# Kernel tuning notes

Hardware: AMD Instinct MI355X
Metric: run time of the kernel (lower is better)

## Reference

```python
import jax, jax.numpy as jnp
import numpy as np
from jax import lax

B, C_IN, N, C_OUT, K = 16, 128, 2048, 256, 20
EPS = 1e-5


def setup_inputs() -> dict:
    key = jax.random.key(0)
    k1, k2 = jax.random.split(key)
    x = jax.random.normal(k1, (B, C_IN, N), dtype=jnp.float32)
    W = jax.random.normal(k2, (C_OUT, 2 * C_IN), dtype=jnp.float32) * (1.0 / np.sqrt(2 * C_IN))
    gamma = jnp.ones((C_OUT,), dtype=jnp.float32)
    beta = jnp.zeros((C_OUT,), dtype=jnp.float32)
    return {"x": x, "W": W, "gamma": gamma, "beta": beta, "k": K}


def _knn_inds(x, k):
    # squared pairwise distance: (B, N, N); computed with no grad (stop_gradient)
    xs = lax.stop_gradient(x)
    inner = jnp.einsum('bcn,bcm->bnm', xs, xs)
    sq = jnp.sum(xs * xs, axis=1)  # (B, N)
    pd = sq[:, :, None] - 2.0 * inner + sq[:, None, :]
    _, inds = lax.top_k(-pd, k)  # smallest distances -> (B, N, k)
    return inds


def reference(x, W, gamma, beta, k):
    knn = _knn_inds(x, k)                                   # (B, N, k) int
    # gather neighbours: neigh[b,c,n,j] = x[b,c,knn[b,n,j]]
    neigh = jax.vmap(lambda xb, kb: xb[:, kb])(x, knn)      # (B, C, N, k)
    central = jnp.broadcast_to(x[:, :, :, None], neigh.shape)
    edge = jnp.concatenate([central, neigh - central], axis=1)  # (B, 2C, N, k)
    # 1x1 conv (bias-free) as GEMM
    y = jnp.einsum('oc,bcnk->bonk', W, edge)                # (B, C_out, N, k)
    # BatchNorm2d (training-mode batch stats) + affine
    mean = jnp.mean(y, axis=(0, 2, 3), keepdims=True)
    var = jnp.var(y, axis=(0, 2, 3), keepdims=True)
    y = (y - mean) * lax.rsqrt(var + EPS)
    y = y * gamma[None, :, None, None] + beta[None, :, None, None]
    y = jax.nn.relu(y)
    return jnp.max(y, axis=3)                               # (B, C_out, N)
```

## Files before the change

### kernel.cpp

```cpp
#include <hip/hip_runtime.h>

#define B_   16
#define CIN  128
#define NPT  2048
#define COUT 256
#define KNN  20
#define KEEP 16
#define CAND 64
#define SIFT 32
#define EPS  1e-5f
#define DBIAS 256.0f

#define SQ_OFF   0ull
#define IDX_OFF  131072ull
#define UT_OFF   2752512ull
#define VT_OFF   36306944ull
#define GS_OFF   69861376ull
#define ST_OFF   69865472ull
#define AMAX_OFF 69871616ull
#define AMIN_OFF 103426048ull
#define WS_NEED_FUSED 136980480ull
#define XT_OFF   UT_OFF
#define XHT_OFF  VT_OFF

typedef _Float16 f16x8 __attribute__((ext_vector_type(8)));
typedef float    f32x4 __attribute__((ext_vector_type(4)));

__global__ __launch_bounds__(256) void prep_kernel(const float* __restrict__ x,
                                                   float* __restrict__ xT,
                                                   _Float16* __restrict__ xhT,
                                                   float* __restrict__ sqh) {
    __shared__ float Ls[128 * 68];
    __shared__ float ps[4 * 64];
    const int b = blockIdx.y, n0 = blockIdx.x * 64, t = threadIdx.x;
    const float* xb = x + (size_t)b * CIN * NPT;
    #pragma unroll
    for (int e = 0; e < 8; ++e) {
        int f = e * 256 + t;
        int c = f >> 4, n4 = (f & 15) << 2;
        *(float4*)&Ls[c * 68 + n4] = *(const float4*)&xb[(size_t)c * NPT + n0 + n4];
    }
    __syncthreads();
    {
        int nl = t & 63, part = t >> 6;
        float acc = 0.f;
        #pragma unroll
        for (int j = 0; j < 32; ++j) {
            float vh = (float)(_Float16)Ls[(part * 32 + j) * 68 + nl];
            acc += vh * vh;
        }
        ps[part * 64 + nl] = acc;
    }
    #pragma unroll
    for (int e = 0; e < 2; ++e) {
        int u = e * 256 + t;
        int nl = u >> 3, ck = (u & 7) << 4;
        float vv[16];
        #pragma unroll
        for (int j = 0; j < 16; ++j) vv[j] = Ls[(ck + j) * 68 + nl];
        size_t row = (size_t)b * NPT + n0 + nl;
        #pragma unroll
        for (int j = 0; j < 4; ++j) {
            float4 w = {vv[4 * j], vv[4 * j + 1], vv[4 * j + 2], vv[4 * j + 3]};
            *(float4*)&xT[row * CIN + ck + 4 * j] = w;
        }
        f16x8 h0, h1;
        #pragma unroll
        for (int j = 0; j < 8; ++j) { h0[j] = (_Float16)vv[j]; h1[j] = (_Float16)vv[8 + j]; }
        *(f16x8*)&xhT[row * CIN + ck] = h0;
        *(f16x8*)&xhT[row * CIN + ck + 8] = h1;
    }
    __syncthreads();
    if (t < 64) sqh[b * NPT + n0 + t] = ps[t] + ps[64 + t] + ps[128 + t] + ps[192 + t];
}

__global__ void wconv_kernel(const float* __restrict__ W,
                             _Float16* __restrict__ Wu,
                             _Float16* __restrict__ Wv) {
    int gid = blockIdx.x * 256 + threadIdx.x;
    int o = gid >> 7, c = gid & 127;
    float w1 = W[o * 256 + c], w2 = W[o * 256 + 128 + c];
    Wu[gid] = (_Float16)(w1 - w2);
    Wv[gid] = (_Float16)w2;
}

__device__ __forceinline__ void stage_pts(const _Float16* __restrict__ xhb,
                                          _Float16* buf, int base_n, int t) {
    const int l15 = t & 15, ks = t >> 6;
    const int quad = (t >> 4) & 3;
    const int c = ks * 32 + quad * 8;
    #pragma unroll
    for (int e = 0; e < 4; ++e) {
        const int n = base_n + e * 16 + l15;
        const _Float16* src = xhb + (size_t)n * CIN + c;
        _Float16* dst = buf + (size_t)(e * 256 + (t & 192)) * 8;
        __builtin_amdgcn_global_load_lds(
            (const __attribute__((address_space(1))) void*)src,
            (__attribute__((address_space(3))) void*)dst, 16, 0, 0);
    }
}

__global__ __launch_bounds__(256, 2) void knn_kernel(const _Float16* __restrict__ xhT,
                                                     const float* __restrict__ xT,
                                                     const float* __restrict__ sqh,
                                                     int* __restrict__ knn_out) {
    __shared__ char smraw[58368];
    _Float16* bufA = (_Float16*)smraw;
    _Float16* bufB = (_Float16*)(smraw + 16384);
    float*    Dt   = (float*)(smraw + 32768);
    float*    sqm  = (float*)(smraw + 50176);

    const int b  = blockIdx.y;
    const int q0 = blockIdx.x * 64;
    const int t  = threadIdx.x;
    const int lane = t & 63, wv = t >> 6;
    const int l15 = lane & 15, quad = lane >> 4;
    const _Float16* xhb = xhT + (size_t)b * NPT * CIN;

    #pragma unroll
    for (int e = 0; e < 8; ++e)
        sqm[e * 256 + t] = sqh[b * NPT + e * 256 + t] + DBIAS;

    stage_pts(xhb, bufA, q0, t);
    __syncthreads();
    f16x8 af[4];
    #pragma unroll
    for (int ks = 0; ks < 4; ++ks)
        af[ks] = *(const f16x8*)(bufA + (size_t)((wv * 4 + ks) * 64 + lane) * 8);
    stage_pts(xhb, bufB, 0, t);

    float bd[KEEP];
    #pragma unroll
    for (int i = 0; i < KEEP; ++i) bd[i] = 3.0e38f;
    const int qi = t >> 2, r = t & 3;

    #pragma unroll 1
    for (int s = 0; s < 32; ++s) {
        __syncthreads();
        _Float16* cur = (s & 1) ? bufA : bufB;
        if (s < 31) stage_pts(xhb, (s & 1) ? bufB : bufA, (s + 1) * 64, t);
        const int m0 = s * 64;
        f32x4 acc[4];
        #pragma unroll
        for (int mt4 = 0; mt4 < 4; ++mt4) acc[mt4] = (f32x4){0.f, 0.f, 0.f, 0.f};
        #pragma unroll
        for (int ks = 0; ks < 4; ++ks) {
            #pragma unroll
            for (int mt4 = 0; mt4 < 4; ++mt4) {
                f16x8 bf = *(const f16x8*)(cur + (size_t)((mt4 * 4 + ks) * 64 + lane) * 8);
                acc[mt4] = __builtin_amdgcn_mfma_f32_16x16x32_f16(af[ks], bf, acc[mt4], 0, 0, 0);
            }
        }
        #pragma unroll
        for (int mt4 = 0; mt4 < 4; ++mt4) {
            float sm_ = sqm[m0 + mt4 * 16 + l15];
            #pragma unroll
            for (int reg = 0; reg < 4; ++reg) {
                int q = wv * 16 + quad * 4 + reg;
                Dt[q * 68 + mt4 * 16 + l15] = sm_ - 2.f * acc[mt4][reg];
            }
        }
        __syncthreads();
        float nk[16];
        #pragma unroll
        for (int i = 0; i < 16; ++i) {
            unsigned bb = __float_as_uint(Dt[qi * 68 + (i << 2) + r]);
            nk[i] = __uint_as_float((bb & 0xFFFFF800u) | (unsigned)(m0 + (i << 2) + r));
        }
        #pragma unroll
        for (int kk = 2; kk <= 16; kk <<= 1) {
            #pragma unroll
            for (int j = kk >> 1; j > 0; j >>= 1) {
                #pragma unroll
                for (int i = 0; i < 16; ++i) {
                    int p = i ^ j;
                    if (p > i) {
                        float a = nk[i], c = nk[p];
                        float lo = fminf(a, c), hi = fmaxf(a, c);
                        if ((i & kk) == 0) { nk[i] = lo; nk[p] = hi; }
                        else               { nk[i] = hi; nk[p] = lo; }
                    }
                }
            }
        }
        #pragma unroll
        for (int i = 0; i < 16; ++i) bd[i] = fminf(bd[i], nk[15 - i]);
        #pragma unroll
        for (int j = 8; j > 0; j >>= 1) {
            #pragma unroll
            for (int i = 0; i < 16; ++i) {
                int p = i ^ j;
                if (p > i) {
                    float a = bd[i], c = bd[p];
                    bd[i] = fminf(a, c);
                    bd[p] = fmaxf(a, c);
                }
            }
        }
    }

    float* Keys = (float*)smraw;
    int*   Surv = (int*)(smraw + 16640);
    double* ddL = (double*)(smraw + 25088);
    #pragma unroll
    for (int i = 0; i < KEEP; ++i)
        Keys[qi * 65 + r * KEEP + i] = bd[i];
    __syncthreads();
    {
        int cnt[KEEP];
        #pragma unroll
        for (int i = 0; i < KEEP; ++i) cnt[i] = 0;
        #pragma unroll 4
        for (int j = 0; j < CAND; ++j) {
            float kj = Keys[qi * 65 + j];
            #pragma unroll
            for (int i = 0; i < KEEP; ++i)
                cnt[i] += (kj < bd[i]) ? 1 : 0;
        }
        __syncthreads();
        #pragma unroll
        for (int i = 0; i < KEEP; ++i)
            if (cnt[i] < SIFT)
                Surv[qi * 33 + cnt[i]] = (int)(__float_as_uint(bd[i]) & 0x7FFu);
    }
    __syncthreads();

    int ms[8];
    #pragma unroll
    for (int k = 0; k < 8; ++k) ms[k] = Surv[qi * 33 + r * 8 + k] & 2047;
    double dd8[8];
    #pragma unroll
    for (int k = 0; k < 8; ++k) dd8[k] = 0.0;
    const float* xTb = xT + (size_t)b * NPT * CIN;
    const float* qrow = xTb + (size_t)(q0 + qi) * CIN;
    #pragma unroll 1
    for (int ch = 0; ch < 8; ++ch) {
        double qd[16];
        #pragma unroll
        for (int j = 0; j < 4; ++j) {
            float4 qv = *(const float4*)&qrow[ch * 16 + 4 * j];
            qd[4 * j] = (double)qv.x; qd[4 * j + 1] = (double)qv.y;
            qd[4 * j + 2] = (double)qv.z; qd[4 * j + 3] = (double)qv.w;
        }
        #pragma unroll
        for (int k = 0; k < 8; ++k) {
            const float* mrow = xTb + (size_t)ms[k] * CIN + ch * 16;
            float4 ma = *(const float4*)&mrow[0];
            float4 mb = *(const float4*)&mrow[4];
            float4 mc = *(const float4*)&mrow[8];
            float4 md = *(const float4*)&mrow[12];
            double ss = dd8[k], d0;
            d0 = qd[0]  - (double)ma.x; ss = fma(d0, d0, ss);
            d0 = qd[1]  - (double)ma.y; ss = fma(d0, d0, ss);
            d0 = qd[2]  - (double)ma.z; ss = fma(d0, d0, ss);
            d0 = qd[3]  - (double)ma.w; ss = fma(d0, d0, ss);
            d0 = qd[4]  - (double)mb.x; ss = fma(d0, d0, ss);
            d0 = qd[5]  - (double)mb.y; ss = fma(d0, d0, ss);
            d0 = qd[6]  - (double)mb.z; ss = fma(d0, d0, ss);
            d0 = qd[7]  - (double)mb.w; ss = fma(d0, d0, ss);
            d0 = qd[8]  - (double)mc.x; ss = fma(d0, d0, ss);
            d0 = qd[9]  - (double)mc.y; ss = fma(d0, d0, ss);
            d0 = qd[10] - (double)mc.z; ss = fma(d0, d0, ss);
            d0 = qd[11] - (double)mc.w; ss = fma(d0, d0, ss);
            d0 = qd[12] - (double)md.x; ss = fma(d0, d0, ss);
            d0 = qd[13] - (double)md.y; ss = fma(d0, d0, ss);
            d0 = qd[14] - (double)md.z; ss = fma(d0, d0, ss);
            d0 = qd[15] - (double)md.w; ss = fma(d0, d0, ss);
            dd8[k] = ss;
        }
    }

    #pragma unroll
    for (int k = 0; k < 8; ++k) ddL[qi * 33 + r * 8 + k] = dd8[k];
    __syncthreads();
    int* dst = knn_out + ((size_t)b * NPT + q0 + qi) * KNN;
    #pragma unroll
    for (int k = 0; k < 8; ++k) {
        int c = 0;
        #pragma unroll 4
        for (int j = 0; j < SIFT; ++j)
            c += (ddL[qi * 33 + j] < dd8[k]) ? 1 : 0;
        if (c < KNN) dst[c] = ms[k];
    }
}

__global__ __launch_bounds__(256) void uv_gemm_h(const _Float16* __restrict__ xhT,
                                                 const _Float16* __restrict__ Wu,
                                                 const _Float16* __restrict__ Wv,
                                                 float* __restrict__ uT,
                                                 float* __restrict__ vT) {
    __shared__ _Float16 Bx[8192];
    const int b = blockIdx.y, n0 = blockIdx.x * 64, t = threadIdx.x;
    const int lane = t & 63, w = t >> 6, l15 = lane & 15, quad = lane >> 4;
    stage_pts(xhT + (size_t)b * NPT * CIN, Bx, n0, t);
    __syncthreads();
    f16x8 bf[4];
    #pragma unroll
    for (int ks = 0; ks < 4; ++ks)
        bf[ks] = *(const f16x8*)(Bx + (size_t)((w * 4 + ks) * 64 + lane) * 8);
    const int n = n0 + w * 16 + l15;
    #pragma unroll 1
    for (int ot = 0; ot < 16; ++ot) {
        const _Float16* wu = Wu + (size_t)(ot * 16 + l15) * 128 + quad * 8;
        const _Float16* wv2 = Wv + (size_t)(ot * 16 + l15) * 128 + quad * 8;
        f32x4 au = (f32x4){0.f, 0.f, 0.f, 0.f};
        f32x4 av = (f32x4){0.f, 0.f, 0.f, 0.f};
        #pragma unroll
        for (int ks = 0; ks < 4; ++ks) {
            f16x8 a_u = *(const f16x8*)(wu + ks * 32);
            f16x8 a_v = *(const f16x8*)(wv2 + ks * 32);
            au = __builtin_amdgcn_mfma_f32_16x16x32_f16(a_u, bf[ks], au, 0, 0, 0);
            av = __builtin_amdgcn_mfma_f32_16x16x32_f16(a_v, bf[ks], av, 0, 0, 0);
        }
        size_t base = ((size_t)b * NPT + n) * COUT + ot * 16 + quad * 4;
        *(f32x4*)&uT[base] = au;
        *(f32x4*)&vT[base] = av;
    }
}

__global__ __launch_bounds__(256) void uv_gemm(const float* __restrict__ x,
                                               const float* __restrict__ W,
                                               float* __restrict__ uT,
                                               float* __restrict__ vT) {
    __shared__ float Ax[32 * 64];
    __shared__ float Bu[32 * 68];
    __shared__ float Bv[32 * 68];
    const int b  = blockIdx.z;
    const int n0 = blockIdx.x * 64;
    const int o0 = blockIdx.y * 64;
    const int t  = threadIdx.x;
    const int tx = t & 15, ty = t >> 4;
    const float* xb = x + (size_t)b * CIN * NPT;
    float au[4][4], av_[4][4];
    #pragma unroll
    for (int i = 0; i < 4; ++i)
        #pragma unroll
        for (int j = 0; j < 4; ++j) { au[i][j] = 0.f; av_[i][j] = 0.f; }
    #pragma unroll 1
    for (int kc = 0; kc < 4; ++kc) {
        const int c0 = kc * 32;
        __syncthreads();
        #pragma unroll
        for (int e = 0; e < 2; ++e) {
            int f = e * 256 + t;
            int cz = f >> 4, ni = (f & 15) << 2;
            *(float4*)&Ax[(cz << 6) + ni] = *(const float4*)&xb[(size_t)(c0 + cz) * NPT + n0 + ni];
        }
        #pragma unroll
        for (int e = 0; e < 8; ++e) {
            int ii = e * 256 + t;
            int cz = ii & 31, oj = ii >> 5;
            float w1 = W[(size_t)(o0 + oj) * 256 + c0 + cz];
            float w2 = W[(size_t)(o0 + oj) * 256 + 128 + c0 + cz];
            Bu[cz * 68 + oj] = w1 - w2;
            Bv[cz * 68 + oj] = w2;
        }
        __syncthreads();
        #pragma unroll 8
        for (int cz = 0; cz < 32; ++cz) {
            const float4 a4 = *(const float4*)&Ax[(cz << 6) + (tx << 2)];
            float bu0 = Bu[cz * 68 + (ty << 2) + 0], bv0 = Bv[cz * 68 + (ty << 2) + 0];
            float bu1 = Bu[cz * 68 + (ty << 2) + 1], bv1 = Bv[cz * 68 + (ty << 2) + 1];
            float bu2 = Bu[cz * 68 + (ty << 2) + 2], bv2 = Bv[cz * 68 + (ty << 2) + 2];
            float bu3 = Bu[cz * 68 + (ty << 2) + 3], bv3 = Bv[cz * 68 + (ty << 2) + 3];
            au[0][0] += a4.x * bu0; au[0][1] += a4.x * bu1; au[0][2] += a4.x * bu2; au[0][3] += a4.x * bu3;
            au[1][0] += a4.y * bu0; au[1][1] += a4.y * bu1; au[1][2] += a4.y * bu2; au[1][3] += a4.y * bu3;
            au[2][0] += a4.z * bu0; au[2][1] += a4.z * bu1; au[2][2] += a4.z * bu2; au[2][3] += a4.z * bu3;
            au[3][0] += a4.w * bu0; au[3][1] += a4.w * bu1; au[3][2] += a4.w * bu2; au[3][3] += a4.w * bu3;
            av_[0][0] += a4.x * bv0; av_[0][1] += a4.x * bv1; av_[0][2] += a4.x * bv2; av_[0][3] += a4.x * bv3;
            av_[1][0] += a4.y * bv0; av_[1][1] += a4.y * bv1; av_[1][2] += a4.y * bv2; av_[1][3] += a4.y * bv3;
            av_[2][0] += a4.z * bv0; av_[2][1] += a4.z * bv1; av_[2][2] += a4.z * bv2; av_[2][3] += a4.z * bv3;
            av_[3][0] += a4.w * bv0; av_[3][1] += a4.w * bv1; av_[3][2] += a4.w * bv2; av_[3][3] += a4.w * bv3;
        }
    }
    #pragma unroll
    for (int i = 0; i < 4; ++i) {
        int n = n0 + (tx << 2) + i;
        size_t base = ((size_t)b * NPT + n) * COUT + o0 + (ty << 2);
        float4 u4 = {au[i][0], au[i][1], au[i][2], au[i][3]};
        float4 v4 = {av_[i][0], av_[i][1], av_[i][2], av_[i][3]};
        *(float4*)&uT[base] = u4;
        *(float4*)&vT[base] = v4;
    }
}

__global__ __launch_bounds__(256) void gather_stats(const float* __restrict__ uT,
                                                    const float* __restrict__ vT,
                                                    const int* __restrict__ knn_in,
                                                    double* __restrict__ gsum,
                                                    float* __restrict__ aMax,
                                                    float* __restrict__ aMin) {
    __shared__ int sidx[16 * KNN];
    const int b  = blockIdx.y;
    const int n0 = blockIdx.x * 64 + blockIdx.z * 16;
    const int o  = threadIdx.x;
    for (int e = o; e < 16 * KNN; e += 256)
        sidx[e] = knn_in[((size_t)b * NPT + n0) * KNN + e];
    __syncthreads();
    const float* ub = uT + ((size_t)b * NPT + n0) * COUT + o;
    const float* vb = vT + (size_t)b * NPT * COUT + o;
    float* amx = aMax + ((size_t)b * NPT + n0) * COUT + o;
    float* amn = aMin + ((size_t)b * NPT + n0) * COUT + o;
    double s1 = 0.0, s2 = 0.0;
    #pragma unroll 1
    for (int s = 0; s < 16; ++s) {
        float u = ub[(size_t)s * COUT];
        float vmax = -3e38f, vmin = 3e38f, vsum = 0.f, vsq = 0.f;
        #pragma unroll
        for (int j = 0; j < KNN; ++j) {
            float v = vb[(size_t)sidx[s * KNN + j] * COUT];
            vmax = fmaxf(vmax, v);
            vmin = fminf(vmin, v);
            vsum += v;
            vsq = fmaf(v, v, vsq);
        }
        s1 += 20.0 * (double)u + (double)vsum;
        s2 += 20.0 * (double)u * (double)u + 2.0 * (double)u * (double)vsum + (double)vsq;
        amx[(size_t)s * COUT] = vmax;
        amn[(size_t)s * COUT] = vmin;
    }
    atomicAdd(&gsum[o], s1);
    atomicAdd(&gsum[COUT + o], s2);
}

__global__ __launch_bounds__(256) void stats_kernel(const float* __restrict__ uT,
                                                    const float* __restrict__ vT,
                                                    const int* __restrict__ knn_in,
                                                    double* __restrict__ gsum) {
    __shared__ int sidx[64 * KNN];
    const int b  = blockIdx.y;
    const int n0 = blockIdx.x * 64;
    const int o  = threadIdx.x;
    for (int e = o; e < 64 * KNN; e += 256)
        sidx[e] = knn_in[((size_t)b * NPT + n0) * KNN + e];
    __syncthreads();
    const float* ub = uT + ((size_t)b * NPT + n0) * COUT + o;
    const float* vb = vT + (size_t)b * NPT * COUT + o;
    double s1 = 0.0, s2 = 0.0;
    #pragma unroll 1
    for (int s = 0; s < 64; ++s) {
        float u = ub[(size_t)s * COUT];
        #pragma unroll
        for (int j = 0; j < KNN; ++j) {
            float y = u + vb[(size_t)sidx[s * KNN + j] * COUT];
            s1 += (double)y;
            s2 = fma((double)y, (double)y, s2);
        }
    }
    atomicAdd(&gsum[o], s1);
    atomicAdd(&gsum[COUT + o], s2);
}

__global__ void finalize_kernel(const double* __restrict__ gsum,
                                const float* __restrict__ gamma,
                                const float* __restrict__ beta,
                                float* __restrict__ st) {
    const int o = threadIdx.x;
    const double M = (double)B_ * NPT * KNN;
    double mean = gsum[o] / M;
    double var  = gsum[COUT + o] / M - mean * mean;
    float inv = 1.0f / sqrtf((float)var + EPS);
    float s = gamma[o] * inv;
    st[o] = s;
    st[COUT + o] = beta[o] - (float)mean * s;
}

__global__ __launch_bounds__(256, 2) void out2_kernel(const float* __restrict__ uT,
                                                      const float* __restrict__ aMax,
                                                      const float* __restrict__ aMin,
                                                      const float* __restrict__ st,
                                                      float* __restrict__ out) {
    __shared__ float zt[256 * 68];
    const int b  = blockIdx.y;
    const int n0 = blockIdx.x * 64;
    const int o  = threadIdx.x;
    const float s  = st[o];
    const float tt = st[COUT + o];
    const float* ub  = uT   + ((size_t)b * NPT + n0) * COUT + o;
    const float* amx = aMax + ((size_t)b * NPT + n0) * COUT + o;
    const float* amn = aMin + ((size_t)b * NPT + n0) * COUT + o;
    #pragma unroll 2
    for (int si = 0; si < 64; ++si) {
        float u = ub[(size_t)si * COUT];
        float y1 = u + amx[(size_t)si * COUT];
        float y2 = u + amn[(size_t)si * COUT];
        float z1 = fmaxf(s * y1 + tt, 0.f);
        float z2 = fmaxf(s * y2 + tt, 0.f);
        zt[o * 68 + si] = fmaxf(z1, z2);
    }
    __syncthreads();
    float* dst = out + ((size_t)b * COUT + o) * NPT + n0;
    #pragma unroll
    for (int i = 0; i < 16; ++i)
        *(float4*)&dst[i * 4] = *(const float4*)&zt[o * 68 + i * 4];
}

__global__ __launch_bounds__(256, 2) void out_kernel(const float* __restrict__ uT,
                                                     const float* __restrict__ vT,
                                                     const int* __restrict__ knn_in,
                                                     const float* __restrict__ st,
                                                     float* __restrict__ out) {
    __shared__ int sidx[64 * KNN];
    __shared__ float zt[256 * 68];
    const int b  = blockIdx.y;
    const int n0 = blockIdx.x * 64;
    const int o  = threadIdx.x;
    for (int e = o; e < 64 * KNN; e += 256)
        sidx[e] = knn_in[((size_t)b * NPT + n0) * KNN + e];
    __syncthreads();
    const float s  = st[o];
    const float tt = st[COUT + o];
    const float* ub = uT + ((size_t)b * NPT + n0) * COUT + o;
    const float* vb = vT + (size_t)b * NPT * COUT + o;
    #pragma unroll 1
    for (int si = 0; si < 64; ++si) {
        float u = ub[(size_t)si * COUT];
        float ymax = -3e38f, ymin = 3e38f;
        #pragma unroll
        for (int j = 0; j < KNN; ++j) {
            float y = u + vb[(size_t)sidx[si * KNN + j] * COUT];
            ymax = fmaxf(ymax, y);
            ymin = fminf(ymin, y);
        }
        float z1 = fmaxf(s * ymax + tt, 0.f);
        float z2 = fmaxf(s * ymin + tt, 0.f);
        zt[o * 68 + si] = fmaxf(z1, z2);
    }
    __syncthreads();
    float* dst = out + ((size_t)b * COUT + o) * NPT + n0;
    #pragma unroll
    for (int i = 0; i < 16; ++i)
        *(float4*)&dst[i * 4] = *(const float4*)&zt[o * 68 + i * 4];
}

extern "C" void kernel_launch(void* const* d_in, const int* in_sizes, int n_in,
                              void* d_out, int out_size, void* d_ws, size_t ws_size,
                              hipStream_t stream) {
    const float* x     = (const float*)d_in[0];
    const float* W     = (const float*)d_in[1];
    const float* gamma = (const float*)d_in[2];
    const float* beta  = (const float*)d_in[3];
    float* out = (float*)d_out;
    char* ws = (char*)d_ws;
    float*     sqh  = (float*)(ws + SQ_OFF);
    int*       idx  = (int*)(ws + IDX_OFF);
    float*     uT   = (float*)(ws + UT_OFF);
    float*     vT   = (float*)(ws + VT_OFF);
    double*    gsum = (double*)(ws + GS_OFF);
    float*     st   = (float*)(ws + ST_OFF);
    float*     aMax = (float*)(ws + AMAX_OFF);
    float*     aMin = (float*)(ws + AMIN_OFF);
    const bool fused = (ws_size >= WS_NEED_FUSED);

    hipMemsetAsync(gsum, 0, 2 * COUT * sizeof(double), stream);
    if (fused) {
        float*    xT  = (float*)(ws + AMAX_OFF);
        _Float16* xhT = (_Float16*)(ws + AMAX_OFF + 16777216ull);
        _Float16* Wu  = (_Float16*)(ws + AMAX_OFF + 25165824ull);
        _Float16* Wv  = (_Float16*)(ws + AMAX_OFF + 25231360ull);
        prep_kernel<<<dim3(32, 16), 256, 0, stream>>>(x, xT, xhT, sqh);
        wconv_kernel<<<128, 256, 0, stream>>>(W, Wu, Wv);
        knn_kernel<<<dim3(32, 16), 256, 0, stream>>>(xhT, xT, sqh, idx);
        uv_gemm_h<<<dim3(32, 16), 256, 0, stream>>>(xhT, Wu, Wv, uT, vT);
        gather_stats<<<dim3(32, 16, 4), 256, 0, stream>>>(uT, vT, idx, gsum, aMax, aMin);
        finalize_kernel<<<1, 256, 0, stream>>>(gsum, gamma, beta, st);
        out2_kernel<<<dim3(32, 16), 256, 0, stream>>>(uT, aMax, aMin, st, out);
    } else {
        float*    xT  = (float*)(ws + XT_OFF);
        _Float16* xhT = (_Float16*)(ws + XHT_OFF);
        prep_kernel<<<dim3(32, 16), 256, 0, stream>>>(x, xT, xhT, sqh);
        knn_kernel<<<dim3(32, 16), 256, 0, stream>>>(xhT, xT, sqh, idx);
        uv_gemm<<<dim3(32, 4, 16), 256, 0, stream>>>(x, W, uT, vT);
        stats_kernel<<<dim3(32, 16), 256, 0, stream>>>(uT, vT, idx, gsum);
        finalize_kernel<<<1, 256, 0, stream>>>(gsum, gamma, beta, st);
        out_kernel<<<dim3(32, 16), 256, 0, stream>>>(uT, vT, idx, st, out);
    }
}
```

Measured before the change: 357.9 us.

## Make KNN distance tiles wave-private to remove block barriers in main loop

Each wave now keeps all 64 query fragments in registers and streams its own 16-candidate slice of points into a private double-buffered LDS region. Distances are written to a per-wave scratch tile, and each lane sorts its own query's 16 candidates. This removes the two __syncthreads per iteration and the shared 64-wide staging. The cost is more registers for the A fragments (64 VGPRs of f16x8), explicit waitcnt and sched barriers, and a changed candidate-to-thread mapping in the merge phase.

After: 352.2 us. Within noise of the previous version (-1.6%).

```diff
diff --git a/kernel.cpp b/kernel.cpp
--- a/kernel.cpp
+++ b/kernel.cpp
@@ -25,6 +25,7 @@
 
 typedef _Float16 f16x8 __attribute__((ext_vector_type(8)));
 typedef float    f32x4 __attribute__((ext_vector_type(4)));
+typedef float    f32x2 __attribute__((ext_vector_type(2)));
 
 __global__ __launch_bounds__(256) void prep_kernel(const float* __restrict__ x,
                                                    float* __restrict__ xT,
@@ -100,15 +101,24 @@
     }
 }
 
+__device__ __forceinline__ void stage_tile16(const _Float16* __restrict__ srcl,
+                                             _Float16* dsthalf) {
+    #pragma unroll
+    for (int e = 0; e < 4; ++e) {
+        __builtin_amdgcn_global_load_lds(
+            (const __attribute__((address_space(1))) void*)(srcl + e * 32),
+            (__attribute__((address_space(3))) void*)(dsthalf + (size_t)e * 512),
+            16, 0, 0);
+    }
+}
+
 __global__ __launch_bounds__(256, 2) void knn_kernel(const _Float16* __restrict__ xhT,
                                                      const float* __restrict__ xT,
                                                      const float* __restrict__ sqh,
                                                      int* __restrict__ knn_out) {
-    __shared__ char smraw[58368];
+    __shared__ char smraw[59392];
     _Float16* bufA = (_Float16*)smraw;
-    _Float16* bufB = (_Float16*)(smraw + 16384);
-    float*    Dt   = (float*)(smraw + 32768);
-    float*    sqm  = (float*)(smraw + 50176);
+    float*    sqm  = (float*)(smraw + 18432);
 
     const int b  = blockIdx.y;
     const int q0 = blockIdx.x * 64;
@@ -123,49 +133,68 @@
 
     stage_pts(xhb, bufA, q0, t);
     __syncthreads();
-    f16x8 af[4];
-    #pragma unroll
-    for (int ks = 0; ks < 4; ++ks)
-        af[ks] = *(const f16x8*)(bufA + (size_t)((wv * 4 + ks) * 64 + lane) * 8);
-    stage_pts(xhb, bufB, 0, t);
+
+    f16x8 af[4][4];
+    #pragma unroll
+    for (int qh = 0; qh < 4; ++qh)
+        #pragma unroll
+        for (int ks = 0; ks < 4; ++ks)
+            af[qh][ks] = *(const f16x8*)(bufA + (size_t)((qh * 4 + ks) * 64 + lane) * 8);
+    __syncthreads();
+
+    _Float16* wbuf = (_Float16*)(smraw + 26624 + wv * 8192);
+    float*    DtW  = (float*)(smraw + wv * 4608);
+    const _Float16* srcl = xhb + (size_t)(wv * 16 + l15) * CIN + quad * 8;
+
+    stage_tile16(srcl, wbuf);
 
     float bd[KEEP];
     #pragma unroll
     for (int i = 0; i < KEEP; ++i) bd[i] = 3.0e38f;
-    const int qi = t >> 2, r = t & 3;
 
     #pragma unroll 1
-    for (int s = 0; s < 32; ++s) {
-        __syncthreads();
-        _Float16* cur = (s & 1) ? bufA : bufB;
-        if (s < 31) stage_pts(xhb, (s & 1) ? bufB : bufA, (s + 1) * 64, t);
-        const int m0 = s * 64;
+    for (int ss = 0; ss < 32; ++ss) {
+        const int mb = ss * 64 + wv * 16;
+        asm volatile("s_waitcnt vmcnt(0)" ::: "memory");
+        __builtin_amdgcn_sched_barrier(0);
+        const _Float16* cur = wbuf + (ss & 1) * 2048;
+        f16x8 bf[4];
+        #pragma unroll
+        for (int ks = 0; ks < 4; ++ks)
+            bf[ks] = *(const f16x8*)(cur + ks * 512 + quad * 128 + l15 * 8);
+        float sm_ = sqm[mb + l15];
+        asm volatile("s_waitcnt lgkmcnt(0)" ::: "memory");
+        __builtin_amdgcn_sched_barrier(0);
+        if (ss < 31)
+            stage_tile16(srcl + (size_t)(ss + 1) * 64 * CIN,
+                         wbuf + ((ss + 1) & 1) * 2048);
+        __builtin_amdgcn_sched_barrier(0);
         f32x4 acc[4];
         #pragma unroll
-        for (int mt4 = 0; mt4 < 4; ++mt4) acc[mt4] = (f32x4){0.f, 0.f, 0.f, 0.f};
-        #pragma unroll
-        for (int ks = 0; ks < 4; ++ks) {
+        for (int qh = 0; qh < 4; ++qh) acc[qh] = (f32x4){0.f, 0.f, 0.f, 0.f};
+        #pragma unroll
+        for (int ks = 0; ks < 4; ++ks)
             #pragma unroll
-            for (int mt4 = 0; mt4 < 4; ++mt4) {
-                f16x8 bf = *(const f16x8*)(cur + (size_t)((mt4 * 4 + ks) * 64 + lane) * 8);
-                acc[mt4] = __builtin_amdgcn_mfma_f32_16x16x32_f16(af[ks], bf, acc[mt4], 0, 0, 0);
+            for (int qh = 0; qh < 4; ++qh)
+                acc[qh] = __builtin_amdgcn_mfma_f32_16x16x32_f16(af[qh][ks], bf[ks], acc[qh], 0, 0, 0);
+        const unsigned om = (unsigned)(mb + l15);
+        #pragma unroll
+        for (int qh = 0; qh < 4; ++qh) {
+            #pragma unroll
+            for (int rg = 0; rg < 4; ++rg) {
+                int q = qh * 16 + quad * 4 + rg;
+                float d = sm_ - 2.f * acc[qh][rg];
+                DtW[q * 18 + l15] = __uint_as_float((__float_as_uint(d) & 0xFFFFF800u) | om);
             }
         }
-        #pragma unroll
-        for (int mt4 = 0; mt4 < 4; ++mt4) {
-            float sm_ = sqm[m0 + mt4 * 16 + l15];
+        float nk[16];
+        {
+            const float* myrow = DtW + lane * 18;
             #pragma unroll
-            for (int reg = 0; reg < 4; ++reg) {
-                int q = wv * 16 + quad * 4 + reg;
-                Dt[q * 68 + mt4 * 16 + l15] = sm_ - 2.f * acc[mt4][reg];
+            for (int p = 0; p < 8; ++p) {
+                f32x2 v = *(const f32x2*)(myrow + 2 * p);
+                nk[2 * p] = v[0]; nk[2 * p + 1] = v[1];
             }
-        }
-        __syncthreads();
-        float nk[16];
-        #pragma unroll
-        for (int i = 0; i < 16; ++i) {
-            unsigned bb = __float_as_uint(Dt[qi * 68 + (i << 2) + r]);
-            nk[i] = __uint_as_float((bb & 0xFFFFF800u) | (unsigned)(m0 + (i << 2) + r));
         }
         #pragma unroll
         for (int kk = 2; kk <= 16; kk <<= 1) {
@@ -199,12 +228,14 @@
         }
     }
 
-    float* Keys = (float*)smraw;
-    int*   Surv = (int*)(smraw + 16640);
-    double* ddL = (double*)(smraw + 25088);
+    __syncthreads();
+
+    float*  Keys = (float*)smraw;
+    int*    Surv = (int*)(smraw + 16640);
+    double* ddL  = (double*)(smraw + 25088);
     #pragma unroll
     for (int i = 0; i < KEEP; ++i)
-        Keys[qi * 65 + r * KEEP + i] = bd[i];
+        Keys[lane * 65 + wv * KEEP + i] = bd[i];
     __syncthreads();
     {
         int cnt[KEEP];
@@ -212,7 +243,7 @@
         for (int i = 0; i < KEEP; ++i) cnt[i] = 0;
         #pragma unroll 4
         for (int j = 0; j < CAND; ++j) {
-            float kj = Keys[qi * 65 + j];
+            float kj = Keys[lane * 65 + j];
             #pragma unroll
             for (int i = 0; i < KEEP; ++i)
                 cnt[i] += (kj < bd[i]) ? 1 : 0;
@@ -221,18 +252,18 @@
         #pragma unroll
         for (int i = 0; i < KEEP; ++i)
             if (cnt[i] < SIFT)
-                Surv[qi * 33 + cnt[i]] = (int)(__float_as_uint(bd[i]) & 0x7FFu);
+                Surv[lane * 33 + cnt[i]] = (int)(__float_as_uint(bd[i]) & 0x7FFu);
     }
     __syncthreads();
 
     int ms[8];
     #pragma unroll
-    for (int k = 0; k < 8; ++k) ms[k] = Surv[qi * 33 + r * 8 + k] & 2047;
+    for (int k = 0; k < 8; ++k) ms[k] = Surv[lane * 33 + wv * 8 + k] & 2047;
     double dd8[8];
     #pragma unroll
     for (int k = 0; k < 8; ++k) dd8[k] = 0.0;
     const float* xTb = xT + (size_t)b * NPT * CIN;
-    const float* qrow = xTb + (size_t)(q0 + qi) * CIN;
+    const float* qrow = xTb + (size_t)(q0 + lane) * CIN;
     #pragma unroll 1
     for (int ch = 0; ch < 8; ++ch) {
         double qd[16];
@@ -246,40 +277,40 @@
         for (int k = 0; k < 8; ++k) {
             const float* mrow = xTb + (size_t)ms[k] * CIN + ch * 16;
             float4 ma = *(const float4*)&mrow[0];
-            float4 mb = *(const float4*)&mrow[4];
+            float4 mb2 = *(const float4*)&mrow[4];
             float4 mc = *(const float4*)&mrow[8];
             float4 md = *(const float4*)&mrow[12];
             double ss = dd8[k], d0;
-            d0 = qd[0]  - (double)ma.x; ss = fma(d0, d0, ss);
-            d0 = qd[1]  - (double)ma.y; ss = fma(d0, d0, ss);
-            d0 = qd[2]  - (double)ma.z; ss = fma(d0, d0, ss);
-            d0 = qd[3]  - (double)ma.w; ss = fma(d0, d0, ss);
-            d0 = qd[4]  - (double)mb.x; ss = fma(d0, d0, ss);
-            d0 = qd[5]  - (double)mb.y; ss = fma(d0, d0, ss);
-            d0 = qd[6]  - (double)mb.z; ss = fma(d0, d0, ss);
-            d0 = qd[7]  - (double)mb.w; ss = fma(d0, d0, ss);
-            d0 = qd[8]  - (double)mc.x; ss = fma(d0, d0, ss);
-            d0 = qd[9]  - (double)mc.y; ss = fma(d0, d0, ss);
-            d0 = qd[10] - (double)mc.z; ss = fma(d0, d0, ss);
-            d0 = qd[11] - (double)mc.w; ss = fma(d0, d0, ss);
-            d0 = qd[12] - (double)md.x; ss = fma(d0, d0, ss);
-            d0 = qd[13] - (double)md.y; ss = fma(d0, d0, ss);
-            d0 = qd[14] - (double)md.z; ss = fma(d0, d0, ss);
-            d0 = qd[15] - (double)md.w; ss = fma(d0, d0, ss);
+            d0 = qd[0]  - (double)ma.x;  ss = fma(d0, d0, ss);
+            d0 = qd[1]  - (double)ma.y;  ss = fma(d0, d0, ss);
+            d0 = qd[2]  - (double)ma.z;  ss = fma(d0, d0, ss);
+            d0 = qd[3]  - (double)ma.w;  ss = fma(d0, d0, ss);
+            d0 = qd[4]  - (double)mb2.x; ss = fma(d0, d0, ss);
+            d0 = qd[5]  - (double)mb2.y; ss = fma(d0, d0, ss);
+            d0 = qd[6]  - (double)mb2.z; ss = fma(d0, d0, ss);
+            d0 = qd[7]  - (double)mb2.w; ss = fma(d0, d0, ss);
+            d0 = qd[8]  - (double)mc.x;  ss = fma(d0, d0, ss);
+            d0 = qd[9]  - (double)mc.y;  ss = fma(d0, d0, ss);
+            d0 = qd[10] - (double)mc.z;  ss = fma(d0, d0, ss);
+            d0 = qd[11] - (double)mc.w;  ss = fma(d0, d0, ss);
+            d0 = qd[12] - (double)md.x;  ss = fma(d0, d0, ss);
+            d0 = qd[13] - (double)md.y;  ss = fma(d0, d0, ss);
+            d0 = qd[14] - (double)md.z;  ss = fma(d0, d0, ss);
+            d0 = qd[15] - (double)md.w;  ss = fma(d0, d0, ss);
             dd8[k] = ss;
         }
     }
 
     #pragma unroll
-    for (int k = 0; k < 8; ++k) ddL[qi * 33 + r * 8 + k] = dd8[k];
-    __syncthreads();
-    int* dst = knn_out + ((size_t)b * NPT + q0 + qi) * KNN;
+    for (int k = 0; k < 8; ++k) ddL[lane * 33 + wv * 8 + k] = dd8[k];
+    __syncthreads();
+    int* dst = knn_out + ((size_t)b * NPT + q0 + lane) * KNN;
     #pragma unroll
     for (int k = 0; k < 8; ++k) {
         int c = 0;
         #pragma unroll 4
         for (int j = 0; j < SIFT; ++j)
-            c += (ddL[qi * 33 + j] < dd8[k]) ? 1 : 0;
+            c += (ddL[lane * 33 + j] < dd8[k]) ? 1 : 0;
         if (c < KNN) dst[c] = ms[k];
     }
 }
```
